# Optimization experiments

Measured on AMD Instinct MI355X. Metric: run time of the kernel, lower is better.

## Reference

```python
import jax, jax.numpy as jnp
import numpy as np

B_SZ = 512; S = 3; F = 5; C = 62; E = 5
D_MODEL = C * E * F          # 1550
N_LAYERS = 2
D_STATE = 16
EXPAND = 2
D_CONV = 4
ED = EXPAND * D_MODEL        # 3100
DT_RANK = (D_MODEL + 15) // 16  # 97
VOCAB = 128
EPS = 1e-5


def setup_inputs() -> dict:
    key = jax.random.key(0)
    ks = jax.random.split(key, 10)
    def g(i, shape, scale=0.02):
        return jax.random.normal(ks[i], shape, dtype=jnp.float32) * scale
    A_log = jnp.tile(jnp.log(jnp.arange(1, D_STATE + 1, dtype=jnp.float32))[None, None, :],
                     (N_LAYERS, ED, 1))
    return {
        "x": jax.random.normal(ks[0], (B_SZ, S, F, C, E), dtype=jnp.float32),
        "in_proj_w": g(1, (N_LAYERS, 2 * ED, D_MODEL)),
        "conv_w": g(2, (N_LAYERS, ED, 1, D_CONV), 0.1),
        "conv_b": jnp.zeros((N_LAYERS, ED), jnp.float32),
        "x_proj_w": g(3, (N_LAYERS, DT_RANK + 2 * D_STATE, ED)),
        "dt_proj_w": g(4, (N_LAYERS, ED, DT_RANK), 0.1),
        "dt_proj_b": jnp.full((N_LAYERS, ED), -4.6, jnp.float32),  # softplus ~ 0.01
        "A_log": A_log,
        "D_param": jnp.ones((N_LAYERS, ED), jnp.float32),
        "out_proj_w": g(5, (N_LAYERS, D_MODEL, ED)),
        "norm_w": jnp.ones((N_LAYERS, D_MODEL), jnp.float32),
        "normf_w": jnp.ones((D_MODEL,), jnp.float32),
        "lm_head_w": g(6, (VOCAB, D_MODEL)),
        "bn_w": jnp.ones((F,), jnp.float32),
        "bn_b": jnp.zeros((F,), jnp.float32),
        "emb_w": g(7, (256, VOCAB)),
        "emb_b": jnp.zeros((256,), jnp.float32),
    }


def _rmsnorm(x, w):
    return x * jax.lax.rsqrt(jnp.mean(x * x, axis=-1, keepdims=True) + EPS) * w


def _silu(x):
    return x * jax.nn.sigmoid(x)


def _causal_conv(xt, w, b):
    # xt: (B, ED, L); w: (ED, 1, K) depthwise causal conv (pad K-1 left)
    y = jax.lax.conv_general_dilated(xt, w, (1,), [(D_CONV - 1, 0)],
                                     feature_group_count=ED)
    return y + b[None, :, None]


def _ssm_scan(deltaA, deltaBx, Cm):
    # deltaA, deltaBx: (B, L, ED, N); Cm: (B, L, N)
    def step(h, inp):
        dA, dBx, c = inp
        h = dA * h + dBx                      # (B, ED, N)
        y = jnp.einsum('ben,bn->be', h, c)    # (B, ED)
        return h, y
    h0 = jnp.zeros((deltaA.shape[0], ED, D_STATE), deltaA.dtype)
    xs = (deltaA.transpose(1, 0, 2, 3), deltaBx.transpose(1, 0, 2, 3), Cm.transpose(1, 0, 2))
    _, ys = jax.lax.scan(step, h0, xs)
    return ys.transpose(1, 0, 2)              # (B, L, ED)


def _mixer(h, in_w, cw, cb, xp_w, dt_w, dt_b, A_log, Dp, out_w):
    # h: (B, L, D_MODEL)
    xz = jnp.einsum('bld,ed->ble', h, in_w)   # (B, L, 2*ED)
    x_in, z = jnp.split(xz, 2, axis=-1)
    xc = _silu(_causal_conv(x_in.transpose(0, 2, 1), cw, cb).transpose(0, 2, 1))  # (B,L,ED)
    dbc = jnp.einsum('ble,re->blr', xc, xp_w)  # (B, L, DT_RANK + 2N)
    dt = dbc[..., :DT_RANK]
    Bm = dbc[..., DT_RANK:DT_RANK + D_STATE]
    Cm = dbc[..., DT_RANK + D_STATE:]
    delta = jax.nn.softplus(jnp.einsum('blr,er->ble', dt, dt_w) + dt_b)  # (B,L,ED)
    A = -jnp.exp(A_log)                       # (ED, N)
    deltaA = jnp.exp(delta[..., None] * A)                       # (B,L,ED,N)
    deltaBx = delta[..., None] * Bm[:, :, None, :] * xc[..., None]
    y = _ssm_scan(deltaA, deltaBx, Cm) + Dp * xc
    return jnp.einsum('ble,de->bld', y * _silu(z), out_w)


def reference(x, in_proj_w, conv_w, conv_b, x_proj_w, dt_proj_w, dt_proj_b,
              A_log, D_param, out_proj_w, norm_w, normf_w, lm_head_w,
              bn_w, bn_b, emb_w, emb_b):
    b, s, f, c, e = x.shape
    fx = x.transpose(0, 1, 3, 2, 4).reshape(b, s, c * f * e)  # (B, S, D_MODEL)
    h = fx
    for l in range(N_LAYERS):
        h = h + _mixer(_rmsnorm(h, norm_w[l]), in_proj_w[l], conv_w[l], conv_b[l],
                       x_proj_w[l], dt_proj_w[l], dt_proj_b[l], A_log[l],
                       D_param[l], out_proj_w[l])
    h = _rmsnorm(h, normf_w)
    logits = jnp.einsum('bsd,vd->bsv', h, lm_head_w)          # (B, S, 128)
    m = jnp.broadcast_to(logits[:, None], (b, f, s, VOCAB))    # repeat over f
    # BatchNorm2d(feature_dim) in training mode: stats over (B, S, VOCAB) per channel f
    mean = jnp.mean(m, axis=(0, 2, 3), keepdims=True)
    var = jnp.var(m, axis=(0, 2, 3), keepdims=True)
    mn = (m - mean) * jax.lax.rsqrt(var + EPS)
    mn = mn * bn_w[None, :, None, None] + bn_b[None, :, None, None]
    return jnp.einsum('bfsv,ov->bfso', mn, emb_w) + emb_b      # (B, F, S, 256)
```

## Files before the change

kernel.cpp:

```cpp
#include <hip/hip_runtime.h>
#include <hip/hip_bf16.h>
#include <math.h>

#define B_SZ 512
#define SEQ 3
#define D_MODEL 1550
#define ED 3100
#define NSTATE 16
#define DTR 97
#define DBC_R 129
#define VOCAB 128
#define NBS (B_SZ*SEQ)
#define EPSV 1e-5f

#define KD 1600
#define KE 3136
#define NIP 6272
#define NXP 256
#define NOP 1664
#define NDT 3200
#define KDT 128
#define DBC_LD 256

#define QIP 2508800
#define QXP 200704
#define QDT 102400
#define QOP 1304576
#define AEL 49600
#define QLM 51200
#define TEL 32768
#define PREP_N1 4166080
#define PREP_N0 4250306

static inline int cdiv_h(int a, int b){ return (a + b - 1) / b; }

__device__ __forceinline__ float silu_f(float x){ return x / (1.0f + expf(-x)); }

using bf16x8 = __attribute__((ext_vector_type(8))) short;
using f32x4  = __attribute__((ext_vector_type(4))) float;

__device__ __forceinline__ void gload16(const void* g, void* l){
  __builtin_amdgcn_global_load_lds(
      (const __attribute__((address_space(1))) unsigned int*)g,
      (__attribute__((address_space(3))) unsigned int*)l,
      16, 0, 0);
}

__device__ __forceinline__ unsigned short bfbits(float v){
  __hip_bfloat16 b = __float2bfloat16(v);
  return *(unsigned short*)&b;
}

__global__ __launch_bounds__(256)
void k_perm_rms(const float* __restrict__ x, const float* __restrict__ w,
                float* __restrict__ h, __hip_bfloat16* __restrict__ hn){
  int row = blockIdx.x;
  const float* xr = x + (size_t)row * D_MODEL;
  float vreg[7]; int dreg[7];
  int cnt = 0;
  float ss = 0.f;
  for (int i = threadIdx.x; i < D_MODEL; i += 256){
    float v = xr[i];
    int e = i % 5, c = (i / 5) % 62, f = i / 310;
    int d = (c * 5 + f) * 5 + e;
    vreg[cnt] = v; dreg[cnt] = d; cnt++;
    ss = fmaf(v, v, ss);
    h[(size_t)row * D_MODEL + d] = v;
  }
  __shared__ float red[4];
  __shared__ float sscale;
  int lane = threadIdx.x & 63, wv = threadIdx.x >> 6;
  #pragma unroll
  for (int o = 32; o > 0; o >>= 1) ss += __shfl_down(ss, o, 64);
  if (lane == 0) red[wv] = ss;
  __syncthreads();
  if (threadIdx.x == 0){
    float t = red[0] + red[1] + red[2] + red[3];
    sscale = 1.0f / sqrtf(t / (float)D_MODEL + EPSV);
  }
  __syncthreads();
  float sc = sscale;
  __hip_bfloat16* orow = hn + (size_t)row * KD;
  for (int k = 0; k < cnt; k++)
    orow[dreg[k]] = __float2bfloat16(vreg[k] * sc * w[dreg[k]]);
  for (int i = D_MODEL + threadIdx.x; i < KD; i += 256)
    orow[i] = __float2bfloat16(0.f);
}

__global__ __launch_bounds__(256)
void k_rms_res(float* __restrict__ h, const __hip_bfloat16* __restrict__ part,
               const float* __restrict__ w, __hip_bfloat16* __restrict__ hn){
  int row = blockIdx.x;
  size_t hb = (size_t)row * D_MODEL;
  float vreg[7];
  int cnt = 0;
  float ss = 0.f;
  for (int i = threadIdx.x; i < D_MODEL; i += 256){
    float v = h[hb + i];
    #pragma unroll
    for (int p = 0; p < 4; p++)
      v += __bfloat162float(part[(size_t)p * NBS * D_MODEL + hb + i]);
    h[hb + i] = v;
    vreg[cnt++] = v;
    ss = fmaf(v, v, ss);
  }
  __shared__ float red[4];
  __shared__ float sscale;
  int lane = threadIdx.x & 63, wv = threadIdx.x >> 6;
  #pragma unroll
  for (int o = 32; o > 0; o >>= 1) ss += __shfl_down(ss, o, 64);
  if (lane == 0) red[wv] = ss;
  __syncthreads();
  if (threadIdx.x == 0){
    float t = red[0] + red[1] + red[2] + red[3];
    sscale = 1.0f / sqrtf(t / (float)D_MODEL + EPSV);
  }
  __syncthreads();
  float sc = sscale;
  __hip_bfloat16* orow = hn + (size_t)row * KD;
  for (int k = 0; k < cnt; k++){
    int i = threadIdx.x + k * 256;
    orow[i] = __float2bfloat16(vreg[k] * sc * w[i]);
  }
  for (int i = D_MODEL + threadIdx.x; i < KD; i += 256)
    orow[i] = __float2bfloat16(0.f);
}

__device__ __forceinline__ void cast4(const float* __restrict__ src,
                                      __hip_bfloat16* __restrict__ dst,
                                      int q, int N, int K, int Kp){
  int i4 = q * 4;
  int row = i4 / Kp;
  int col = i4 % Kp;
  const float* srow = src + (size_t)row * K;
  ushort4 o;
  o.x = bfbits((row < N && col + 0 < K) ? srow[col + 0] : 0.f);
  o.y = bfbits((row < N && col + 1 < K) ? srow[col + 1] : 0.f);
  o.z = bfbits((row < N && col + 2 < K) ? srow[col + 2] : 0.f);
  o.w = bfbits((row < N && col + 3 < K) ? srow[col + 3] : 0.f);
  *(ushort4*)(dst + i4) = o;
}

__global__ __launch_bounds__(256)
void k_prep(const float* __restrict__ ipw, const float* __restrict__ xpw,
            const float* __restrict__ dtw, const float* __restrict__ opw,
            const float* __restrict__ alog,
            const float* __restrict__ lmw, const float* __restrict__ embw,
            __hip_bfloat16* __restrict__ ipb, __hip_bfloat16* __restrict__ xpb,
            __hip_bfloat16* __restrict__ dtwb, __hip_bfloat16* __restrict__ opb,
            float* __restrict__ A_t,
            __hip_bfloat16* __restrict__ lmb,
            float* __restrict__ emb_t, float* __restrict__ sumw,
            float* __restrict__ stats, int l0){
  int idx = blockIdx.x * 256 + threadIdx.x;
  if (idx < QIP){ cast4(ipw, ipb, idx, 2 * ED, D_MODEL, KD); return; } idx -= QIP;
  if (idx < QXP){ cast4(xpw, xpb, idx, DBC_R, ED, KE); return; } idx -= QXP;
  if (idx < QDT){ cast4(dtw, dtwb, idx, ED, DTR, KDT); return; } idx -= QDT;
  if (idx < QOP){ cast4(opw, opb, idx, D_MODEL, ED, KE); return; } idx -= QOP;
  if (idx < AEL){
    int n = idx / ED, ch = idx % ED;
    A_t[idx] = -expf(alog[(size_t)ch * NSTATE + n]);
    return;
  } idx -= AEL;
  if (!l0) return;
  if (idx < QLM){ cast4(lmw, lmb, idx, VOCAB, D_MODEL, KD); return; } idx -= QLM;
  if (idx < TEL){
    int v = idx >> 8, o = idx & 255;
    emb_t[idx] = embw[(size_t)o * VOCAB + v];
    return;
  } idx -= TEL;
  if (idx < 256){
    const float* r = embw + (size_t)idx * VOCAB;
    float s = 0.f;
    for (int v = 0; v < VOCAB; v++) s += r[v];
    sumw[idx] = s;
    return;
  } idx -= 256;
  if (idx < 2) stats[idx] = 0.f;
}

template<int SPLITS, bool OUT_BF16, bool PARTIAL, bool DUAL>
__global__ __launch_bounds__(256)
void k_gemm2(const __hip_bfloat16* __restrict__ A, const __hip_bfloat16* __restrict__ B,
             void* Cv, void* Cv1, int Kp, int Nld, int Nreal){
  __shared__ short Al[2][4096];
  __shared__ short Bl[2][4096];
  const int gx = gridDim.x, gy = gridDim.y;
  const int nwg = gx * gy;
  const int wg = blockIdx.y * gx + blockIdx.x;
  const int q = nwg >> 3, r = nwg & 7;
  const int xcd = wg & 7, off = wg >> 3;
  const int nid = (xcd < r ? xcd * (q + 1) : r * (q + 1) + (xcd - r) * q) + off;
  const int bm = (nid % gy) * 128;
  const int bn = (nid / gy) * 128;

  const int t = threadIdx.x;
  const int tt8 = t * 8;

  int kb = 0, ke = Kp;
  if (SPLITS > 1){
    int Kc = ((Kp / SPLITS + 31) / 32) * 32;
    kb = blockIdx.z * Kc;
    ke = min(kb + Kc, Kp);
    if (kb >= ke) return;
  }
  const int nt = (ke - kb) / 32;

  const int cg = ((t & 3) ^ ((t >> 2) & 3)) * 8;
  const short* Ab = (const short*)A;
  const short* Bb = (const short*)B;
  const short* ga0 = Ab + (size_t)(bm + (t >> 2)) * Kp + cg;
  const short* ga1 = Ab + (size_t)(bm + 64 + (t >> 2)) * Kp + cg;
  const short* gb0 = Bb + (size_t)(bn + (t >> 2)) * Kp + cg;
  const short* gb1 = Bb + (size_t)(bn + 64 + (t >> 2)) * Kp + cg;

  const int l = t & 63;
  const int wid = t >> 6;
  const int wr = wid >> 1, wc = wid & 1;
  const int fr = l & 15;
  const int cc = ((l >> 4) ^ (l & 3)) * 8;

  f32x4 acc[4][4] = {};

#define STAGE(buf, kof) do{ \
    gload16(ga0 + (kof), &Al[buf][tt8]); \
    gload16(ga1 + (kof), &Al[buf][2048 + tt8]); \
    gload16(gb0 + (kof), &Bl[buf][tt8]); \
    gload16(gb1 + (kof), &Bl[buf][2048 + tt8]); }while(0)

  STAGE(0, kb);
  __syncthreads();
  int cur = 0;
  for (int it = 0; it < nt; ++it){
    if (it + 1 < nt) STAGE(cur ^ 1, kb + (it + 1) * 32);
    bf16x8 af[4], bfr[4];
    #pragma unroll
    for (int m = 0; m < 4; m++)
      af[m] = *(const bf16x8*)&Al[cur][(wr * 64 + m * 16 + fr) * 32 + cc];
    #pragma unroll
    for (int n = 0; n < 4; n++)
      bfr[n] = *(const bf16x8*)&Bl[cur][(wc * 64 + n * 16 + fr) * 32 + cc];
    #pragma unroll
    for (int m = 0; m < 4; m++)
      #pragma unroll
      for (int n = 0; n < 4; n++)
        acc[m][n] = __builtin_amdgcn_mfma_f32_16x16x32_bf16(af[m], bfr[n], acc[m][n], 0, 0, 0);
    if (it + 1 < nt){ __syncthreads(); cur ^= 1; }
  }
#undef STAGE

  float* Cf = (float*)Cv;
  __hip_bfloat16* Cb = (__hip_bfloat16*)Cv;
  if (DUAL && blockIdx.z == 1) Cb = (__hip_bfloat16*)Cv1;
  if (PARTIAL){
    const size_t pstride = (size_t)gy * 128 * Nld;
    if (OUT_BF16) Cb += (size_t)blockIdx.z * pstride;
    else          Cf += (size_t)blockIdx.z * pstride;
  }
  const int r0 = (l >> 4) * 4;
  #pragma unroll
  for (int m = 0; m < 4; m++){
    #pragma unroll
    for (int n = 0; n < 4; n++){
      int col = bn + wc * 64 + n * 16 + fr;
      if (col < Nreal){
        size_t base = (size_t)(bm + wr * 64 + m * 16 + r0) * Nld + col;
        #pragma unroll
        for (int j = 0; j < 4; j++){
          float v = acc[m][n][j];
          size_t o = base + (size_t)j * Nld;
          if (OUT_BF16) Cb[o] = __float2bfloat16(v);
          else          Cf[o] = v;
        }
      }
    }
  }
}

__global__ void k_conv_silu2(__hip_bfloat16* __restrict__ xz0,
                             const __hip_bfloat16* __restrict__ xz1,
                             const float* __restrict__ cw, const float* __restrict__ cb,
                             __hip_bfloat16* __restrict__ xc_b){
  int idx = blockIdx.x * 256 + threadIdx.x;
  if (idx >= B_SZ * KE) return;
  int ch = idx % KE;
  int b  = idx / KE;
  size_t ob = (size_t)b * SEQ * KE + ch;
  if (ch >= ED){
    __hip_bfloat16 z = __float2bfloat16(0.f);
    xc_b[ob] = z; xc_b[ob + KE] = z; xc_b[ob + 2 * KE] = z;
    return;
  }
  size_t rb = (size_t)b * SEQ * NIP;
  const __hip_bfloat16* p0 = xz0 + rb + ch;
  const __hip_bfloat16* p1 = xz1 + rb + ch;
  float x0 = __bfloat162float(p0[0])       + __bfloat162float(p1[0]);
  float x1 = __bfloat162float(p0[NIP])     + __bfloat162float(p1[NIP]);
  float x2 = __bfloat162float(p0[2 * NIP]) + __bfloat162float(p1[2 * NIP]);
  __hip_bfloat16* q0 = xz0 + rb + ED + ch;
  const __hip_bfloat16* q1 = xz1 + rb + ED + ch;
  #pragma unroll
  for (int t = 0; t < SEQ; t++){
    float zv = __bfloat162float(q0[(size_t)t * NIP]) + __bfloat162float(q1[(size_t)t * NIP]);
    q0[(size_t)t * NIP] = __float2bfloat16(zv);
  }
  const float* w = cw + (size_t)ch * 4;
  float w1 = w[1], w2 = w[2], w3 = w[3];
  float bb = cb[ch];
  float s0 = silu_f(fmaf(w3, x0, bb));
  float s1 = silu_f(fmaf(w2, x0, fmaf(w3, x1, bb)));
  float s2 = silu_f(fmaf(w1, x0, fmaf(w2, x1, fmaf(w3, x2, bb))));
  xc_b[ob]          = __float2bfloat16(s0);
  xc_b[ob + KE]     = __float2bfloat16(s1);
  xc_b[ob + 2 * KE] = __float2bfloat16(s2);
}

__global__ __launch_bounds__(256)
void k_xred(const float* __restrict__ part, float* __restrict__ dbc,
            __hip_bfloat16* __restrict__ dbc_b){
  int idx = blockIdx.x * 256 + threadIdx.x;
  if (idx >= NBS * DBC_LD) return;
  float s = 0.f;
  #pragma unroll
  for (int p = 0; p < 8; p++) s += part[(size_t)p * NBS * DBC_LD + idx];
  dbc[idx] = s;
  int c = idx & 255, row = idx >> 8;
  if (c < KDT) dbc_b[(size_t)row * KDT + c] = __float2bfloat16(c < DTR ? s : 0.f);
}

__global__ __launch_bounds__(256)
void k_scan2(const __hip_bfloat16* __restrict__ delta_b, const float* __restrict__ dbc,
             const float* __restrict__ dtb, const float* __restrict__ A_t,
             const float* __restrict__ Dp, const __hip_bfloat16* __restrict__ xz,
             __hip_bfloat16* __restrict__ xc_b){
  __shared__ float sB[SEQ][NSTATE], sC[SEQ][NSTATE];
  int b = blockIdx.y;
  if (threadIdx.x < SEQ * 2 * NSTATE){
    int t = threadIdx.x / (2 * NSTATE), r = threadIdx.x % (2 * NSTATE);
    float v = dbc[(size_t)(b * SEQ + t) * DBC_LD + DTR + r];
    if (r < NSTATE) sB[t][r] = v; else sC[t][r - NSTATE] = v;
  }
  __syncthreads();
  int ch = blockIdx.x * 256 + threadIdx.x;
  if (ch >= ED) return;

  float bias = dtb[ch];
  float dlt[SEQ];
  #pragma unroll
  for (int t = 0; t < SEQ; t++){
    float acc = __bfloat162float(delta_b[(size_t)(b * SEQ + t) * NDT + ch]) + bias;
    dlt[t] = (acc > 20.f) ? acc : log1pf(expf(acc));
  }

  size_t ob = (size_t)b * SEQ * KE + ch;
  float xcv[SEQ] = { __bfloat162float(xc_b[ob]),
                     __bfloat162float(xc_b[ob + KE]),
                     __bfloat162float(xc_b[ob + 2 * KE]) };
  float y[SEQ] = {0.f, 0.f, 0.f};
  #pragma unroll
  for (int n = 0; n < NSTATE; n++){
    float Av = A_t[(size_t)n * ED + ch];
    float hs = 0.f;
    #pragma unroll
    for (int t = 0; t < SEQ; t++){
      float dA = expf(dlt[t] * Av);
      hs = fmaf(dA, hs, dlt[t] * sB[t][n] * xcv[t]);
      y[t] = fmaf(hs, sC[t][n], y[t]);
    }
  }
  float dp = Dp[ch];
  const __hip_bfloat16* zbase = xz + (size_t)b * SEQ * NIP + ED + ch;
  #pragma unroll
  for (int t = 0; t < SEQ; t++){
    float z = __bfloat162float(zbase[(size_t)t * NIP]);
    float yy = fmaf(dp, xcv[t], y[t]);
    xc_b[ob + (size_t)t * KE] = __float2bfloat16(yy * silu_f(z));
  }
}

__global__ __launch_bounds__(256)
void k_statsred(const float* __restrict__ part, float* __restrict__ logits,
                float* __restrict__ stats){
  float s = 0.f, ss = 0.f;
  for (int i = blockIdx.x * 256 + threadIdx.x; i < NBS * VOCAB; i += gridDim.x * 256){
    float v = 0.f;
    #pragma unroll
    for (int p = 0; p < 4; p++) v += part[(size_t)p * NBS * VOCAB + i];
    logits[i] = v;
    s += v; ss = fmaf(v, v, ss);
  }
  #pragma unroll
  for (int o = 32; o > 0; o >>= 1){ s += __shfl_down(s, o, 64); ss += __shfl_down(ss, o, 64); }
  __shared__ float rs[4], rss[4];
  int lane = threadIdx.x & 63, wv = threadIdx.x >> 6;
  if (lane == 0){ rs[wv] = s; rss[wv] = ss; }
  __syncthreads();
  if (threadIdx.x == 0){
    atomicAdd(&stats[0], rs[0] + rs[1] + rs[2] + rs[3]);
    atomicAdd(&stats[1], rss[0] + rss[1] + rss[2] + rss[3]);
  }
}

__global__ __launch_bounds__(256)
void k_projfinal(const float* __restrict__ logits, const float* __restrict__ emb_t,
                 const float* __restrict__ sumw, const float* __restrict__ stats,
                 const float* __restrict__ bnw, const float* __restrict__ bnb,
                 const float* __restrict__ embb, float* __restrict__ out){
  __shared__ float row[VOCAB];
  int r = blockIdx.x;
  int o = threadIdx.x;
  if (o < VOCAB) row[o] = logits[(size_t)r * VOCAB + o];
  __syncthreads();
  float p = 0.f;
  #pragma unroll 8
  for (int v = 0; v < VOCAB; v++) p = fmaf(row[v], emb_t[v * 256 + o], p);
  const float invN = 1.0f / (float)(NBS * VOCAB);
  float mean = stats[0] * invN;
  float var  = stats[1] * invN - mean * mean;
  float rstd = rsqrtf(var + EPSV);
  int b = r / SEQ, s = r % SEQ;
  float sw = sumw[o];
  float base = rstd * (p - mean * sw);
  float eb = embb[o];
  #pragma unroll
  for (int f = 0; f < 5; f++){
    out[(((size_t)(b * 5 + f)) * SEQ + s) * 256 + o] = bnw[f] * base + bnb[f] * sw + eb;
  }
}

extern "C" void kernel_launch(void* const* d_in, const int* in_sizes, int n_in,
                              void* d_out, int out_size, void* d_ws, size_t ws_size,
                              hipStream_t stream) {
  const float* x          = (const float*)d_in[0];
  const float* in_proj_w  = (const float*)d_in[1];
  const float* conv_w     = (const float*)d_in[2];
  const float* conv_b     = (const float*)d_in[3];
  const float* x_proj_w   = (const float*)d_in[4];
  const float* dt_proj_w  = (const float*)d_in[5];
  const float* dt_proj_b  = (const float*)d_in[6];
  const float* A_log      = (const float*)d_in[7];
  const float* D_param    = (const float*)d_in[8];
  const float* out_proj_w = (const float*)d_in[9];
  const float* norm_w     = (const float*)d_in[10];
  const float* normf_w    = (const float*)d_in[11];
  const float* lm_head_w  = (const float*)d_in[12];
  const float* bn_w       = (const float*)d_in[13];
  const float* bn_b       = (const float*)d_in[14];
  const float* emb_w      = (const float*)d_in[15];
  const float* emb_b      = (const float*)d_in[16];

  float* ws = (float*)d_ws;
  float* h      = ws;
  float* dbc    = h      + (size_t)NBS * D_MODEL;
  float* logits = dbc    + (size_t)NBS * DBC_LD;
  float* sumw   = logits + (size_t)NBS * VOCAB;
  float* stats  = sumw   + 256;
  float* A_t    = stats  + 2;
  float* emb_t  = A_t    + (size_t)NSTATE * ED;
  float* spart  = emb_t  + (size_t)VOCAB * 256;
  size_t spart_f = (size_t)NBS * NIP / 2;
  float* xpart  = spart;
  float* lmpart = spart;
  __hip_bfloat16* opart = (__hip_bfloat16*)spart;
  __hip_bfloat16* ipz1  = (__hip_bfloat16*)spart;
  __hip_bfloat16* xz_b   = (__hip_bfloat16*)(spart + spart_f);
  __hip_bfloat16* hn_b   = xz_b   + (size_t)NBS * NIP;
  __hip_bfloat16* xc_b   = hn_b   + (size_t)NBS * KD;
  __hip_bfloat16* dbc_b  = xc_b   + (size_t)NBS * KE;
  __hip_bfloat16* dlt_b  = dbc_b  + (size_t)NBS * KDT;
  __hip_bfloat16* ipb    = dlt_b  + (size_t)NBS * NDT;
  __hip_bfloat16* xpb    = ipb    + (size_t)NIP * KD;
  __hip_bfloat16* dtwb   = xpb    + (size_t)NXP * KE;
  __hip_bfloat16* opb    = dtwb   + (size_t)NDT * KDT;
  __hip_bfloat16* lmb    = opb    + (size_t)NOP * KE;
  size_t need = (size_t)((char*)(lmb + (size_t)VOCAB * KD) - (char*)ws);
  if (ws_size < need) return;

  for (int l = 0; l < 2; l++){
    const float* ipw = in_proj_w  + (size_t)l * 2 * ED * D_MODEL;
    const float* cw  = conv_w     + (size_t)l * ED * 4;
    const float* cb  = conv_b     + (size_t)l * ED;
    const float* xpw = x_proj_w   + (size_t)l * DBC_R * ED;
    const float* dtw = dt_proj_w  + (size_t)l * ED * DTR;
    const float* dtb = dt_proj_b  + (size_t)l * ED;
    const float* al  = A_log      + (size_t)l * ED * NSTATE;
    const float* dp  = D_param    + (size_t)l * ED;
    const float* opw = out_proj_w + (size_t)l * D_MODEL * ED;
    const float* nw  = norm_w     + (size_t)l * D_MODEL;

    k_prep<<<cdiv_h(l == 0 ? PREP_N0 : PREP_N1, 256), 256, 0, stream>>>(
        ipw, xpw, dtw, opw, al, lm_head_w, emb_w,
        ipb, xpb, dtwb, opb, A_t, lmb, emb_t, sumw, stats, l == 0 ? 1 : 0);

    if (l == 0){
      k_perm_rms<<<NBS, 256, 0, stream>>>(x, nw, h, hn_b);
    } else {
      k_rms_res<<<NBS, 256, 0, stream>>>(h, opart, nw, hn_b);
    }

    k_gemm2<2, true, false, true><<<dim3(NIP / 128, NBS / 128, 2), 256, 0, stream>>>(
        hn_b, ipb, xz_b, ipz1, KD, NIP, NIP);

    k_conv_silu2<<<cdiv_h(B_SZ * KE, 256), 256, 0, stream>>>(xz_b, ipz1, cw, cb, xc_b);

    k_gemm2<8, false, true, false><<<dim3(NXP / 128, NBS / 128, 8), 256, 0, stream>>>(
        xc_b, xpb, xpart, nullptr, KE, DBC_LD, DBC_LD);
    k_xred<<<cdiv_h(NBS * DBC_LD, 256), 256, 0, stream>>>(xpart, dbc, dbc_b);

    k_gemm2<1, true, false, false><<<dim3(NDT / 128, NBS / 128, 1), 256, 0, stream>>>(
        dbc_b, dtwb, dlt_b, nullptr, KDT, NDT, NDT);

    k_scan2<<<dim3(cdiv_h(ED, 256), B_SZ), 256, 0, stream>>>(
        dlt_b, dbc, dtb, A_t, dp, xz_b, xc_b);

    k_gemm2<4, true, true, false><<<dim3(NOP / 128, NBS / 128, 4), 256, 0, stream>>>(
        xc_b, opb, opart, nullptr, KE, D_MODEL, D_MODEL);
  }

  k_rms_res<<<NBS, 256, 0, stream>>>(h, opart, normf_w, hn_b);
  k_gemm2<4, false, true, false><<<dim3(1, NBS / 128, 4), 256, 0, stream>>>(
      hn_b, lmb, lmpart, nullptr, KD, VOCAB, VOCAB);
  k_statsred<<<192, 256, 0, stream>>>(lmpart, logits, stats);

  k_projfinal<<<NBS, 256, 0, stream>>>(logits, emb_t, sumw, stats,
                                       bn_w, bn_b, emb_b, (float*)d_out);
}
```

Baseline: 492.1 us.

## Triple-buffer GEMM LDS pipeline and drop split-K for in_proj

The bf16 MFMA GEMM goes from a double-buffered to a triple-buffered LDS pipeline. Loads are issued two stages ahead and gated with an explicit vmcnt wait plus one barrier per iteration, replacing the two __syncthreads per iteration. The in_proj GEMM no longer splits K into two partial outputs, so conv_silu reads one buffer and skips the add-and-write-back of the z half. The cost is more LDS per block and fewer workgroups for in_proj, with twice the K loop length per block.

Result: faster. 480.6 us (-2.3%).

```diff
diff --git a/kernel.cpp b/kernel.cpp
--- a/kernel.cpp
+++ b/kernel.cpp
@@ -179,12 +179,12 @@
   if (idx < 2) stats[idx] = 0.f;
 }
 
-template<int SPLITS, bool OUT_BF16, bool PARTIAL, bool DUAL>
-__global__ __launch_bounds__(256)
-void k_gemm2(const __hip_bfloat16* __restrict__ A, const __hip_bfloat16* __restrict__ B,
-             void* Cv, void* Cv1, int Kp, int Nld, int Nreal){
-  __shared__ short Al[2][4096];
-  __shared__ short Bl[2][4096];
+template<int SPLITS, bool OUT_BF16, bool PARTIAL>
+__global__ __launch_bounds__(256)
+void k_gemm3(const __hip_bfloat16* __restrict__ A, const __hip_bfloat16* __restrict__ B,
+             void* Cv, int Kp, int Nld, int Nreal){
+  __shared__ short Al[3][4096];
+  __shared__ short Bl[3][4096];
   const int gx = gridDim.x, gy = gridDim.y;
   const int nwg = gx * gy;
   const int wg = blockIdx.y * gx + blockIdx.x;
@@ -229,29 +229,34 @@
     gload16(gb1 + (kof), &Bl[buf][2048 + tt8]); }while(0)
 
   STAGE(0, kb);
-  __syncthreads();
-  int cur = 0;
+  if (nt > 1) STAGE(1, kb + 32);
+  int bsel = 0, snext = 2;
   for (int it = 0; it < nt; ++it){
-    if (it + 1 < nt) STAGE(cur ^ 1, kb + (it + 1) * 32);
+    if (it + 1 < nt) asm volatile("s_waitcnt vmcnt(4)" ::: "memory");
+    else             asm volatile("s_waitcnt vmcnt(0)" ::: "memory");
+    __builtin_amdgcn_s_barrier();
+    asm volatile("" ::: "memory");
+    __builtin_amdgcn_sched_barrier(0);
+    if (it + 2 < nt) STAGE(snext, kb + (it + 2) * 32);
     bf16x8 af[4], bfr[4];
     #pragma unroll
     for (int m = 0; m < 4; m++)
-      af[m] = *(const bf16x8*)&Al[cur][(wr * 64 + m * 16 + fr) * 32 + cc];
+      af[m] = *(const bf16x8*)&Al[bsel][(wr * 64 + m * 16 + fr) * 32 + cc];
     #pragma unroll
     for (int n = 0; n < 4; n++)
-      bfr[n] = *(const bf16x8*)&Bl[cur][(wc * 64 + n * 16 + fr) * 32 + cc];
+      bfr[n] = *(const bf16x8*)&Bl[bsel][(wc * 64 + n * 16 + fr) * 32 + cc];
     #pragma unroll
     for (int m = 0; m < 4; m++)
       #pragma unroll
       for (int n = 0; n < 4; n++)
         acc[m][n] = __builtin_amdgcn_mfma_f32_16x16x32_bf16(af[m], bfr[n], acc[m][n], 0, 0, 0);
-    if (it + 1 < nt){ __syncthreads(); cur ^= 1; }
+    bsel = (bsel == 2) ? 0 : bsel + 1;
+    snext = (snext == 2) ? 0 : snext + 1;
   }
 #undef STAGE
 
   float* Cf = (float*)Cv;
   __hip_bfloat16* Cb = (__hip_bfloat16*)Cv;
-  if (DUAL && blockIdx.z == 1) Cb = (__hip_bfloat16*)Cv1;
   if (PARTIAL){
     const size_t pstride = (size_t)gy * 128 * Nld;
     if (OUT_BF16) Cb += (size_t)blockIdx.z * pstride;
@@ -277,10 +282,8 @@
   }
 }
 
-__global__ void k_conv_silu2(__hip_bfloat16* __restrict__ xz0,
-                             const __hip_bfloat16* __restrict__ xz1,
-                             const float* __restrict__ cw, const float* __restrict__ cb,
-                             __hip_bfloat16* __restrict__ xc_b){
+__global__ void k_conv_silu(const __hip_bfloat16* __restrict__ xz, const float* __restrict__ cw,
+                            const float* __restrict__ cb, __hip_bfloat16* __restrict__ xc_b){
   int idx = blockIdx.x * 256 + threadIdx.x;
   if (idx >= B_SZ * KE) return;
   int ch = idx % KE;
@@ -291,19 +294,10 @@
     xc_b[ob] = z; xc_b[ob + KE] = z; xc_b[ob + 2 * KE] = z;
     return;
   }
-  size_t rb = (size_t)b * SEQ * NIP;
-  const __hip_bfloat16* p0 = xz0 + rb + ch;
-  const __hip_bfloat16* p1 = xz1 + rb + ch;
-  float x0 = __bfloat162float(p0[0])       + __bfloat162float(p1[0]);
-  float x1 = __bfloat162float(p0[NIP])     + __bfloat162float(p1[NIP]);
-  float x2 = __bfloat162float(p0[2 * NIP]) + __bfloat162float(p1[2 * NIP]);
-  __hip_bfloat16* q0 = xz0 + rb + ED + ch;
-  const __hip_bfloat16* q1 = xz1 + rb + ED + ch;
-  #pragma unroll
-  for (int t = 0; t < SEQ; t++){
-    float zv = __bfloat162float(q0[(size_t)t * NIP]) + __bfloat162float(q1[(size_t)t * NIP]);
-    q0[(size_t)t * NIP] = __float2bfloat16(zv);
-  }
+  const __hip_bfloat16* base = xz + (size_t)b * SEQ * NIP + ch;
+  float x0 = __bfloat162float(base[0]);
+  float x1 = __bfloat162float(base[NIP]);
+  float x2 = __bfloat162float(base[2 * NIP]);
   const float* w = cw + (size_t)ch * 4;
   float w1 = w[1], w2 = w[2], w3 = w[3];
   float bb = cb[ch];
@@ -458,11 +452,10 @@
   float* A_t    = stats  + 2;
   float* emb_t  = A_t    + (size_t)NSTATE * ED;
   float* spart  = emb_t  + (size_t)VOCAB * 256;
-  size_t spart_f = (size_t)NBS * NIP / 2;
+  size_t spart_f = ((size_t)4 * NBS * D_MODEL * 2 + 3) / 4;
   float* xpart  = spart;
   float* lmpart = spart;
   __hip_bfloat16* opart = (__hip_bfloat16*)spart;
-  __hip_bfloat16* ipz1  = (__hip_bfloat16*)spart;
   __hip_bfloat16* xz_b   = (__hip_bfloat16*)(spart + spart_f);
   __hip_bfloat16* hn_b   = xz_b   + (size_t)NBS * NIP;
   __hip_bfloat16* xc_b   = hn_b   + (size_t)NBS * KD;
@@ -498,28 +491,28 @@
       k_rms_res<<<NBS, 256, 0, stream>>>(h, opart, nw, hn_b);
     }
 
-    k_gemm2<2, true, false, true><<<dim3(NIP / 128, NBS / 128, 2), 256, 0, stream>>>(
-        hn_b, ipb, xz_b, ipz1, KD, NIP, NIP);
-
-    k_conv_silu2<<<cdiv_h(B_SZ * KE, 256), 256, 0, stream>>>(xz_b, ipz1, cw, cb, xc_b);
-
-    k_gemm2<8, false, true, false><<<dim3(NXP / 128, NBS / 128, 8), 256, 0, stream>>>(
-        xc_b, xpb, xpart, nullptr, KE, DBC_LD, DBC_LD);
+    k_gemm3<1, true, false><<<dim3(NIP / 128, NBS / 128, 1), 256, 0, stream>>>(
+        hn_b, ipb, xz_b, KD, NIP, NIP);
+
+    k_conv_silu<<<cdiv_h(B_SZ * KE, 256), 256, 0, stream>>>(xz_b, cw, cb, xc_b);
+
+    k_gemm3<8, false, true><<<dim3(NXP / 128, NBS / 128, 8), 256, 0, stream>>>(
+        xc_b, xpb, xpart, KE, DBC_LD, DBC_LD);
     k_xred<<<cdiv_h(NBS * DBC_LD, 256), 256, 0, stream>>>(xpart, dbc, dbc_b);
 
-    k_gemm2<1, true, false, false><<<dim3(NDT / 128, NBS / 128, 1), 256, 0, stream>>>(
-        dbc_b, dtwb, dlt_b, nullptr, KDT, NDT, NDT);
+    k_gemm3<1, true, false><<<dim3(NDT / 128, NBS / 128, 1), 256, 0, stream>>>(
+        dbc_b, dtwb, dlt_b, KDT, NDT, NDT);
 
     k_scan2<<<dim3(cdiv_h(ED, 256), B_SZ), 256, 0, stream>>>(
         dlt_b, dbc, dtb, A_t, dp, xz_b, xc_b);
 
-    k_gemm2<4, true, true, false><<<dim3(NOP / 128, NBS / 128, 4), 256, 0, stream>>>(
-        xc_b, opb, opart, nullptr, KE, D_MODEL, D_MODEL);
+    k_gemm3<4, true, true><<<dim3(NOP / 128, NBS / 128, 4), 256, 0, stream>>>(
+        xc_b, opb, opart, KE, D_MODEL, D_MODEL);
   }
 
   k_rms_res<<<NBS, 256, 0, stream>>>(h, opart, normf_w, hn_b);
-  k_gemm2<4, false, true, false><<<dim3(1, NBS / 128, 4), 256, 0, stream>>>(
-      hn_b, lmb, lmpart, nullptr, KD, VOCAB, VOCAB);
+  k_gemm3<4, false, true><<<dim3(1, NBS / 128, 4), 256, 0, stream>>>(
+      hn_b, lmb, lmpart, KD, VOCAB, VOCAB);
   k_statsred<<<192, 256, 0, stream>>>(lmpart, logits, stats);
 
   k_projfinal<<<NBS, 256, 0, stream>>>(logits, emb_t, sumw, stats,
```
